# Kernel tuning notes

Measured on AMD Instinct MI355X. Metric: run time of the kernel, lower is better.

The kernel has to match this reference:

```python
import jax, jax.numpy as jnp
import numpy as np

VOCAB, HIDDEN, BATCH, SEQ = 32000, 512, 64, 512


def setup_inputs() -> dict:
    key = jax.random.key(0)
    k0, k1, k2, k3, k4, k5 = jax.random.split(key, 6)
    s = 1.0 / np.sqrt(HIDDEN)  # PyTorch LSTMCell init scale
    return {
        "inputs": jax.random.randint(k0, (BATCH, SEQ), 0, VOCAB, dtype=jnp.int64),
        "embedding": jax.random.normal(k1, (VOCAB, HIDDEN), dtype=jnp.float32),
        "W_ih": jax.random.normal(k2, (4 * HIDDEN, HIDDEN), dtype=jnp.float32) * s,
        "W_hh": jax.random.normal(k3, (4 * HIDDEN, HIDDEN), dtype=jnp.float32) * s,
        "b_ih": jax.random.normal(k4, (4 * HIDDEN,), dtype=jnp.float32) * s,
        "b_hh": jax.random.normal(k5, (4 * HIDDEN,), dtype=jnp.float32) * s,
    }


def reference(inputs, embedding, W_ih, W_hh, b_ih, b_hh):
    # Embedding lookup: (B, S, H)
    x = embedding[inputs]
    B, S, H = x.shape
    bias = b_ih + b_hh

    def step(carry, xt):
        h, c = carry
        # gates: (B, 4H); PyTorch LSTMCell gate order i, f, g, o
        gates = xt @ W_ih.T + h @ W_hh.T + bias
        i, f, g, o = jnp.split(gates, 4, axis=-1)
        i = jax.nn.sigmoid(i)
        f = jax.nn.sigmoid(f)
        g = jnp.tanh(g)
        o = jax.nn.sigmoid(o)
        c_new = f * c + i * g
        h_new = o * jnp.tanh(c_new)
        return (h_new, c_new), h_new

    h0 = jnp.zeros((B, H), dtype=x.dtype)
    c0 = jnp.zeros((B, H), dtype=x.dtype)
    (h, c), hs = jax.lax.scan(step, (h0, c0), jnp.swapaxes(x, 0, 1))
    annotations = jnp.swapaxes(hs, 0, 1)  # (B, S, H)
    return annotations, h, c
```

## Files before the change

kernel.cpp:

```cpp
#include <hip/hip_runtime.h>
#include <math.h>

#define B 64
#define S 512
#define H 512
#define G4 2048

typedef __attribute__((ext_vector_type(8))) short bf16x8;
typedef __attribute__((ext_vector_type(4))) float f32x4;

__device__ __forceinline__ float sigmoidf_(float x) {
    return 1.0f / (1.0f + __expf(-x));
}
__device__ __forceinline__ float tanhf_(float x) {
    return 2.0f / (1.0f + __expf(-2.0f * x)) - 1.0f;
}

__device__ __forceinline__ ushort f2bf(float f) {
    union { float f; unsigned int u; } v; v.f = f;
    unsigned int r = v.u + 0x7FFFu + ((v.u >> 16) & 1u);
    return (ushort)(r >> 16);
}
__device__ __forceinline__ float bf2f(ushort s) {
    union { unsigned int u; float f; } v; v.u = ((unsigned int)s) << 16;
    return v.f;
}
__device__ __forceinline__ void split_bf(float x, ushort& hi, ushort& lo) {
    const ushort h = f2bf(x);
    hi = h;
    lo = f2bf(x - bf2f(h));
}

__global__ __launch_bounds__(256)
void w_split(const float* __restrict__ W,
             ushort* __restrict__ Whi,
             ushort* __restrict__ Wlo)
{
    const int i = blockIdx.x * 256 + threadIdx.x;
    const float4 v = reinterpret_cast<const float4*>(W)[i];
    ushort4 hi, lo;
    split_bf(v.x, hi.x, lo.x);
    split_bf(v.y, hi.y, lo.y);
    split_bf(v.z, hi.z, lo.z);
    split_bf(v.w, hi.w, lo.w);
    reinterpret_cast<ushort4*>(Whi)[i] = hi;
    reinterpret_cast<ushort4*>(Wlo)[i] = lo;
}

__global__ __launch_bounds__(256)
void xg_mfma(const int* __restrict__ tokens,
             const float* __restrict__ emb,
             const ushort* __restrict__ Whi,
             const ushort* __restrict__ Wlo,
             const float* __restrict__ b_ih,
             const float* __restrict__ b_hh,
             ushort* __restrict__ xg)
{
    const int mtile = blockIdx.x;
    const int ntile = blockIdx.y;
    const int tid   = threadIdx.x;

    __shared__ ushort Ahi[128][32];
    __shared__ ushort Alo[128][32];
    __shared__ ushort Bhi[128][32];
    __shared__ ushort Blo[128][32];

    const int ar  = tid >> 3;
    const int seg = tid & 7;
    const float* asrc[4];
    #pragma unroll
    for (int i = 0; i < 4; ++i) {
        const int m   = mtile * 128 + ar + i * 32;
        const int tok = tokens[(m & 63) * S + (m >> 6)];
        asrc[i] = emb + (size_t)tok * H + seg * 4;
    }

    const int br = tid >> 2;
    const int bc = (tid & 3) * 8;
    const ushort* bsrc_hi[2];
    const ushort* bsrc_lo[2];
    #pragma unroll
    for (int j = 0; j < 2; ++j) {
        const int n = ntile * 128 + br + j * 64;
        bsrc_hi[j] = Whi + (size_t)n * H + bc;
        bsrc_lo[j] = Wlo + (size_t)n * H + bc;
    }

    const int lane = tid & 63;
    const int wv   = tid >> 6;
    const int wr   = (wv >> 1) * 64;
    const int wc   = (wv & 1) * 64;
    const int fr   = lane & 15;
    const int ks   = lane >> 4;

    f32x4 acc[4][4];
    #pragma unroll
    for (int a = 0; a < 4; ++a)
        #pragma unroll
        for (int c = 0; c < 4; ++c)
            acc[a][c] = (f32x4){0.f, 0.f, 0.f, 0.f};

    for (int kc = 0; kc < 16; ++kc) {
        const int d0 = kc * 32;

        #pragma unroll
        for (int i = 0; i < 4; ++i) {
            const float4 v = *reinterpret_cast<const float4*>(asrc[i] + d0);
            ushort4 hi, lo;
            split_bf(v.x, hi.x, lo.x);
            split_bf(v.y, hi.y, lo.y);
            split_bf(v.z, hi.z, lo.z);
            split_bf(v.w, hi.w, lo.w);
            const int r = ar + i * 32;
            *reinterpret_cast<ushort4*>(&Ahi[r][seg * 4]) = hi;
            *reinterpret_cast<ushort4*>(&Alo[r][seg * 4]) = lo;
        }
        #pragma unroll
        for (int j = 0; j < 2; ++j) {
            const int r = br + j * 64;
            *reinterpret_cast<uint4*>(&Bhi[r][bc]) =
                *reinterpret_cast<const uint4*>(bsrc_hi[j] + d0);
            *reinterpret_cast<uint4*>(&Blo[r][bc]) =
                *reinterpret_cast<const uint4*>(bsrc_lo[j] + d0);
        }
        __syncthreads();

        bf16x8 ah[4], al[4];
        #pragma unroll
        for (int fm = 0; fm < 4; ++fm) {
            ah[fm] = *reinterpret_cast<const bf16x8*>(&Ahi[wr + fm * 16 + fr][ks * 8]);
            al[fm] = *reinterpret_cast<const bf16x8*>(&Alo[wr + fm * 16 + fr][ks * 8]);
        }
        #pragma unroll
        for (int fn = 0; fn < 4; ++fn) {
            const bf16x8 bh = *reinterpret_cast<const bf16x8*>(&Bhi[wc + fn * 16 + fr][ks * 8]);
            const bf16x8 bl = *reinterpret_cast<const bf16x8*>(&Blo[wc + fn * 16 + fr][ks * 8]);
            #pragma unroll
            for (int fm = 0; fm < 4; ++fm) {
                acc[fm][fn] = __builtin_amdgcn_mfma_f32_16x16x32_bf16(ah[fm], bh, acc[fm][fn], 0, 0, 0);
                acc[fm][fn] = __builtin_amdgcn_mfma_f32_16x16x32_bf16(al[fm], bh, acc[fm][fn], 0, 0, 0);
                acc[fm][fn] = __builtin_amdgcn_mfma_f32_16x16x32_bf16(ah[fm], bl, acc[fm][fn], 0, 0, 0);
            }
        }
        __syncthreads();
    }

    #pragma unroll
    for (int fn = 0; fn < 4; ++fn) {
        const int col  = ntile * 128 + wc + fn * 16 + fr;
        const float bias = b_ih[col] + b_hh[col];
        const int gate = col >> 9;
        const int k    = col & 511;
        const int w    = k >> 4;
        const int kl   = k & 15;
        #pragma unroll
        for (int fm = 0; fm < 4; ++fm) {
            const int row = mtile * 128 + wr + fm * 16 + ks * 4;
            const int t   = row >> 6;
            const int b   = row & 63;
            const int g   = b >> 3;
            const int b8  = b & 7;
            ushort4 us;
            us.x = f2bf(acc[fm][fn][0] + bias);
            us.y = f2bf(acc[fm][fn][1] + bias);
            us.z = f2bf(acc[fm][fn][2] + bias);
            us.w = f2bf(acc[fm][fn][3] + bias);
            const size_t idx = ((((size_t)t * 8 + g) * 32 + w) * 512) +
                               gate * 128 + kl * 8 + b8;
            *reinterpret_cast<ushort4*>(&xg[idx]) = us;
        }
    }
}

__global__ __launch_bounds__(256)
void xg_gemm(const int* __restrict__ tokens,
             const float* __restrict__ emb,
             const float* __restrict__ W_ih,
             const float* __restrict__ b_ih,
             const float* __restrict__ b_hh,
             ushort* __restrict__ xg)
{
    const int t      = blockIdx.x;
    const int g_base = blockIdx.y * 128;
    const int tid    = threadIdx.x;

    const int b_ld = tid >> 2;
    const int seg  = tid & 3;
    const int r_w  = tid >> 1;
    const int half = tid & 1;
    const int b0 = (tid & 15) * 4;
    const int g0 = (tid >> 4) * 8;

    const int token = tokens[b_ld * S + t];
    const float4* embrow = reinterpret_cast<const float4*>(emb) + (size_t)token * (H / 4);

    __shared__ float hs[64][64];
    __shared__ float ws[128][68];

    float acc[4][8];
    #pragma unroll
    for (int i = 0; i < 4; ++i)
        #pragma unroll
        for (int j = 0; j < 8; ++j) acc[i][j] = 0.0f;

    for (int kc = 0; kc < 8; ++kc) {
        const int d0 = kc * 64;
        #pragma unroll
        for (int i = 0; i < 4; ++i) {
            const int dl = seg * 16 + i * 4;
            const float4 f = embrow[(d0 >> 2) + seg * 4 + i];
            hs[dl + 0][b_ld] = f.x;
            hs[dl + 1][b_ld] = f.y;
            hs[dl + 2][b_ld] = f.z;
            hs[dl + 3][b_ld] = f.w;
        }
        const float4* wrow = reinterpret_cast<const float4*>(W_ih) +
                             (size_t)(g_base + r_w) * (H / 4) + (d0 >> 2) + half * 8;
        #pragma unroll
        for (int i = 0; i < 8; ++i) {
            *reinterpret_cast<float4*>(&ws[r_w][half * 32 + i * 4]) = wrow[i];
        }
        __syncthreads();

        #pragma unroll
        for (int d4 = 0; d4 < 16; ++d4) {
            const float4 hv0 = *reinterpret_cast<const float4*>(&hs[d4 * 4 + 0][b0]);
            const float4 hv1 = *reinterpret_cast<const float4*>(&hs[d4 * 4 + 1][b0]);
            const float4 hv2 = *reinterpret_cast<const float4*>(&hs[d4 * 4 + 2][b0]);
            const float4 hv3 = *reinterpret_cast<const float4*>(&hs[d4 * 4 + 3][b0]);
            #pragma unroll
            for (int gg = 0; gg < 8; ++gg) {
                const float4 w = *reinterpret_cast<const float4*>(&ws[g0 + gg][d4 * 4]);
                acc[0][gg] += hv0.x * w.x + hv1.x * w.y + hv2.x * w.z + hv3.x * w.w;
                acc[1][gg] += hv0.y * w.x + hv1.y * w.y + hv2.y * w.z + hv3.y * w.w;
                acc[2][gg] += hv0.z * w.x + hv1.z * w.y + hv2.z * w.z + hv3.z * w.w;
                acc[3][gg] += hv0.w * w.x + hv1.w * w.y + hv2.w * w.z + hv3.w * w.w;
            }
        }
        __syncthreads();
    }

    const int grp = b0 >> 3;
    const int b8l = b0 & 7;
    #pragma unroll
    for (int gg = 0; gg < 8; ++gg) {
        const int gcol = g_base + g0 + gg;
        const int gate = gcol >> 9;
        const int k    = gcol & 511;
        const int w    = k >> 4;
        const int kl   = k & 15;
        const float bias = b_ih[gcol] + b_hh[gcol];
        ushort4 us;
        us.x = f2bf(acc[0][gg] + bias);
        us.y = f2bf(acc[1][gg] + bias);
        us.z = f2bf(acc[2][gg] + bias);
        us.w = f2bf(acc[3][gg] + bias);
        const size_t idx = ((((size_t)t * 8 + grp) * 32 + w) * 512) +
                           gate * 128 + kl * 8 + b8l;
        *reinterpret_cast<ushort4*>(&xg[idx]) = us;
    }
}

#define GSTR 4096
#define PSTR 32768

__global__ __launch_bounds__(256)
__attribute__((amdgpu_waves_per_eu(1, 1)))
void lstm_persist_mfma(const ushort* __restrict__ Whh_hi,
                       const ushort* __restrict__ Whh_lo,
                       const ushort* __restrict__ xg,
                       float* __restrict__ hq,
                       unsigned int* __restrict__ bar,
                       float* __restrict__ out)
{
    const int tid  = threadIdx.x;
    const int g    = blockIdx.x & 7;
    const int w    = blockIdx.x >> 3;
    const int k0   = w * 16;
    const int lane = tid & 63;
    const int wv   = tid >> 6;

    unsigned int* bcnt = bar + g * 64;

    const int  bcol   = lane & 15;
    const int  klane  = 4 * wv + (lane >> 4);
    const bool active = bcol < 8;
    const int  b8     = lane & 7;

    const ushort* xg_wg = xg + (((size_t)g * 32 + w) * 512);

    const int ar    = lane & 15;
    const int agate = ar & 3;
    const int ak    = k0 + 4 * wv + (ar >> 2);
    const size_t arow = ((size_t)agate * 512 + ak) * 512 + (size_t)(lane >> 4) * 8;
    bf16x8 afh[16], afl[16];
    #pragma unroll
    for (int ks = 0; ks < 16; ++ks) {
        afh[ks] = *reinterpret_cast<const bf16x8*>(Whh_hi + arow + ks * 32);
        afl[ks] = *reinterpret_cast<const bf16x8*>(Whh_lo + arow + ks * 32);
    }

    __shared__ ushort hs_hi[8 * 512];
    __shared__ ushort hs_lo[8 * 512];

    float c_reg = 0.0f;

    float xv_cur[4] = {0.f, 0.f, 0.f, 0.f};
    if (active) {
        #pragma unroll
        for (int gate = 0; gate < 4; ++gate)
            xv_cur[gate] = bf2f(xg_wg[gate * 128 + klane * 8 + b8]);
    }

    char* hs_hi_c = reinterpret_cast<char*>(hs_hi);
    char* hs_lo_c = reinterpret_cast<char*>(hs_lo);

    for (int t = 0; t < S; ++t) {
        const unsigned long long* hsrc8 = reinterpret_cast<const unsigned long long*>(
            hq + (t & 1) * PSTR + g * GSTR);
        unsigned long long hv[8];
        #pragma unroll
        for (int i = 0; i < 8; ++i)
            hv[i] = __hip_atomic_load(&hsrc8[i * 256 + tid],
                                      __ATOMIC_RELAXED, __HIP_MEMORY_SCOPE_AGENT);
        #pragma unroll
        for (int i = 0; i < 8; ++i) {
            const int e  = 2 * (i * 256 + tid);
            const int bb = e >> 9;
            const int dd = e & 511;
            union { unsigned long long u; float f[2]; } uv; uv.u = hv[i];
            ushort h0, l0, h1, l1;
            split_bf(uv.f[0], h0, l0);
            split_bf(uv.f[1], h1, l1);
            const int byteoff = ((bb << 10) + (dd << 1)) ^ (bb << 4);
            *reinterpret_cast<unsigned int*>(hs_hi_c + byteoff) =
                ((unsigned int)h1 << 16) | (unsigned int)h0;
            *reinterpret_cast<unsigned int*>(hs_lo_c + byteoff) =
                ((unsigned int)l1 << 16) | (unsigned int)l0;
        }
        __syncthreads();

        float xv_nxt[4] = {0.f, 0.f, 0.f, 0.f};
        if (active && t + 1 < S) {
            const ushort* p = xg_wg + (size_t)(t + 1) * (8 * 32 * 512);
            #pragma unroll
            for (int gate = 0; gate < 4; ++gate)
                xv_nxt[gate] = bf2f(p[gate * 128 + klane * 8 + b8]);
        }

        f32x4 a0 = (f32x4){0.f,0.f,0.f,0.f}, a1 = a0, a2 = a0, a3 = a0, a4 = a0, a5 = a0;
        #pragma unroll
        for (int ks = 0; ks < 16; ++ks) {
            const int kbyte = ((b8 << 10) + ((ks * 32 + (lane >> 4) * 8) << 1)) ^ (b8 << 4);
            const bf16x8 bh = *reinterpret_cast<const bf16x8*>(hs_hi_c + kbyte);
            const bf16x8 bl = *reinterpret_cast<const bf16x8*>(hs_lo_c + kbyte);
            if (ks & 1) {
                a1 = __builtin_amdgcn_mfma_f32_16x16x32_bf16(afh[ks], bh, a1, 0, 0, 0);
                a3 = __builtin_amdgcn_mfma_f32_16x16x32_bf16(afl[ks], bh, a3, 0, 0, 0);
                a5 = __builtin_amdgcn_mfma_f32_16x16x32_bf16(afh[ks], bl, a5, 0, 0, 0);
            } else {
                a0 = __builtin_amdgcn_mfma_f32_16x16x32_bf16(afh[ks], bh, a0, 0, 0, 0);
                a2 = __builtin_amdgcn_mfma_f32_16x16x32_bf16(afl[ks], bh, a2, 0, 0, 0);
                a4 = __builtin_amdgcn_mfma_f32_16x16x32_bf16(afh[ks], bl, a4, 0, 0, 0);
            }
        }
        const f32x4 acc = (a0 + a1) + ((a2 + a3) + (a4 + a5));

        float hn = 0.0f, cn = 0.0f;
        if (active) {
            const float ig = sigmoidf_(acc[0] + xv_cur[0]);
            const float fg = sigmoidf_(acc[1] + xv_cur[1]);
            const float gg = tanhf_(acc[2] + xv_cur[2]);
            const float og = sigmoidf_(acc[3] + xv_cur[3]);
            cn = fg * c_reg + ig * gg;
            c_reg = cn;
            hn = og * tanhf_(cn);
            __hip_atomic_store(&hq[((t & 1) ^ 1) * PSTR + g * GSTR + b8 * 512 + k0 + klane],
                               hn, __ATOMIC_RELAXED, __HIP_MEMORY_SCOPE_AGENT);
        }

        __syncthreads();
        if (tid == 0)
            __hip_atomic_fetch_add(bcnt, 1u, __ATOMIC_RELAXED,
                                   __HIP_MEMORY_SCOPE_AGENT);

        if (active) {
            out[((size_t)(g * 8 + b8) * S + t) * H + k0 + klane] = hn;
            if (t == S - 1) {
                const size_t OFF = (size_t)B * S * H;
                out[OFF + (size_t)(g * 8 + b8) * H + k0 + klane] = hn;
                out[OFF + (size_t)B * H + (size_t)(g * 8 + b8) * H + k0 + klane] = cn;
            }
        }

        const unsigned int target = 32u * (unsigned int)(t + 1);
        while (__hip_atomic_load(bcnt, __ATOMIC_RELAXED,
                                 __HIP_MEMORY_SCOPE_AGENT) < target)
            __builtin_amdgcn_s_sleep(2);

        xv_cur[0] = xv_nxt[0]; xv_cur[1] = xv_nxt[1];
        xv_cur[2] = xv_nxt[2]; xv_cur[3] = xv_nxt[3];
    }
}

__global__ __launch_bounds__(256)
__attribute__((amdgpu_waves_per_eu(1, 1)))
void lstm_persist(const float* __restrict__ W_hh,
                  const ushort* __restrict__ xg,
                  float* __restrict__ hq,
                  unsigned int* __restrict__ bar,
                  float* __restrict__ out)
{
    const int tid = threadIdx.x;
    const int g   = blockIdx.x & 7;
    const int w   = blockIdx.x >> 3;
    const int k0  = w * 16;

    const int rp = tid & 31;
    const int d8 = tid >> 5;
    const int d0 = d8 * 64;

    const int b8 = tid >> 4;
    const int kl = tid & 15;

    unsigned int* bcnt = bar + g * 64;

    const ushort* xg_wg = xg + (((size_t)g * 32 + w) * 512);

    float4 wreg[2][16];
    #pragma unroll
    for (int r = 0; r < 2; ++r) {
        const int rl = 2 * rp + r;
        const int grow = (rl >> 4) * H + k0 + (rl & 15);
        const float4* wp = reinterpret_cast<const float4*>(W_hh + (size_t)grow * H + d0);
        #pragma unroll
        for (int i = 0; i < 16; ++i) wreg[r][i] = wp[i];
    }

    __shared__ float hs[8 * 512];
    __shared__ float part[8 * 8 * 64];

    float c_reg = 0.0f;

    float xv_cur[4] = {0.f, 0.f, 0.f, 0.f};
    if (tid < 128) {
        #pragma unroll
        for (int gate = 0; gate < 4; ++gate)
            xv_cur[gate] = bf2f(xg_wg[gate * 128 + kl * 8 + b8]);
    }

    for (int t = 0; t < S; ++t) {
        const unsigned long long* hsrc8 = reinterpret_cast<const unsigned long long*>(
            hq + (t & 1) * PSTR + g * GSTR);
        #pragma unroll
        for (int i = 0; i < 8; ++i) {
            const unsigned long long v = __hip_atomic_load(&hsrc8[i * 256 + tid],
                                                           __ATOMIC_RELAXED,
                                                           __HIP_MEMORY_SCOPE_AGENT);
            reinterpret_cast<unsigned long long*>(hs)[i * 256 + tid] = v;
        }
        __syncthreads();

        float xv_nxt[4] = {0.f, 0.f, 0.f, 0.f};
        if (tid < 128 && t + 1 < S) {
            const ushort* p = xg_wg + (size_t)(t + 1) * (8 * 32 * 512);
            #pragma unroll
            for (int gate = 0; gate < 4; ++gate)
                xv_nxt[gate] = bf2f(p[gate * 128 + kl * 8 + b8]);
        }

        float acc[2][8];
        #pragma unroll
        for (int r = 0; r < 2; ++r)
            #pragma unroll
            for (int b = 0; b < 8; ++b) acc[r][b] = 0.0f;

        #pragma unroll
        for (int b = 0; b < 8; ++b) {
            const float4* h4 = reinterpret_cast<const float4*>(hs + b * 512 + d0);
            #pragma unroll
            for (int i = 0; i < 16; ++i) {
                const float4 hv = h4[i];
                acc[0][b] += wreg[0][i].x * hv.x + wreg[0][i].y * hv.y +
                             wreg[0][i].z * hv.z + wreg[0][i].w * hv.w;
                acc[1][b] += wreg[1][i].x * hv.x + wreg[1][i].y * hv.y +
                             wreg[1][i].z * hv.z + wreg[1][i].w * hv.w;
            }
        }

        #pragma unroll
        for (int r = 0; r < 2; ++r)
            #pragma unroll
            for (int b = 0; b < 8; ++b)
                part[d8 * 512 + b * 64 + 2 * rp + r] = acc[r][b];
        __syncthreads();

        if (tid < 128) {
            float v[4];
            #pragma unroll
            for (int gate = 0; gate < 4; ++gate) {
                const int rl = gate * 16 + kl;
                float s = 0.0f;
                #pragma unroll
                for (int q = 0; q < 8; ++q) s += part[q * 512 + b8 * 64 + rl];
                v[gate] = s + xv_cur[gate];
            }
            const float ig = sigmoidf_(v[0]);
            const float fg = sigmoidf_(v[1]);
            const float gg = tanhf_(v[2]);
            const float og = sigmoidf_(v[3]);

            const float cn = fg * c_reg + ig * gg;
            c_reg = cn;
            const float hn = og * tanhf_(cn);

            __hip_atomic_store(&hq[((t & 1) ^ 1) * PSTR + g * GSTR + b8 * 512 + k0 + kl],
                               hn, __ATOMIC_RELAXED, __HIP_MEMORY_SCOPE_AGENT);
            out[((size_t)(g * 8 + b8) * S + t) * H + k0 + kl] = hn;
            if (t == S - 1) {
                const size_t OFF = (size_t)B * S * H;
                out[OFF + (size_t)(g * 8 + b8) * H + k0 + kl] = hn;
                out[OFF + (size_t)B * H + (size_t)(g * 8 + b8) * H + k0 + kl] = cn;
            }
        }

        __syncthreads();
        if (tid == 0) {
            __hip_atomic_fetch_add(bcnt, 1u, __ATOMIC_RELAXED,
                                   __HIP_MEMORY_SCOPE_AGENT);
            const unsigned int target = 32u * (unsigned int)(t + 1);
            while (__hip_atomic_load(bcnt, __ATOMIC_RELAXED,
                                     __HIP_MEMORY_SCOPE_AGENT) < target)
                __builtin_amdgcn_s_sleep(2);
        }
        __syncthreads();

        xv_cur[0] = xv_nxt[0]; xv_cur[1] = xv_nxt[1];
        xv_cur[2] = xv_nxt[2]; xv_cur[3] = xv_nxt[3];
    }
}

__global__ __launch_bounds__(128)
void lstm_step_fb(const int* __restrict__ tokens,
                  const float* __restrict__ emb,
                  const float* __restrict__ W_ih,
                  const float* __restrict__ W_hh,
                  const float* __restrict__ b_ih,
                  const float* __restrict__ b_hh,
                  const float* __restrict__ h_prev,
                  float* __restrict__ h_next,
                  float* __restrict__ c_st,
                  float* __restrict__ out,
                  int t)
{
    const int tid = threadIdx.x;
    const int b   = tid & 63;
    const int k   = blockIdx.x * 2 + (tid >> 6);
    const int token = tokens[b * S + t];
    const float* xrow = emb + (size_t)token * H;
    const float* hrow = h_prev + b * H;
    float acc[4];
    #pragma unroll
    for (int g = 0; g < 4; ++g) acc[g] = b_ih[g * H + k] + b_hh[g * H + k];
    for (int d = 0; d < H; ++d) {
        const float xv = xrow[d], hv = hrow[d];
        #pragma unroll
        for (int g = 0; g < 4; ++g)
            acc[g] += xv * W_ih[(size_t)(g * H + k) * H + d] + hv * W_hh[(size_t)(g * H + k) * H + d];
    }
    const float ig = sigmoidf_(acc[0]);
    const float fg = sigmoidf_(acc[1]);
    const float gg = tanhf(acc[2]);
    const float og = sigmoidf_(acc[3]);
    const int ck = b * H + k;
    const float cn = fg * c_st[ck] + ig * gg;
    c_st[ck] = cn;
    const float hn = og * tanhf(cn);
    h_next[ck] = hn;
    out[(size_t)b * S * H + (size_t)t * H + k] = hn;
    if (t == S - 1) {
        out[(size_t)B * S * H + ck] = hn;
        out[(size_t)B * S * H + B * H + ck] = cn;
    }
}

extern "C" void kernel_launch(void* const* d_in, const int* in_sizes, int n_in,
                              void* d_out, int out_size, void* d_ws, size_t ws_size,
                              hipStream_t stream)
{
    const int*   tokens = (const int*)d_in[0];
    const float* emb    = (const float*)d_in[1];
    const float* W_ih   = (const float*)d_in[2];
    const float* W_hh   = (const float*)d_in[3];
    const float* b_ih   = (const float*)d_in[4];
    const float* b_hh   = (const float*)d_in[5];
    float* out = (float*)d_out;

    const size_t XG_BYTES  = (size_t)S * G4 * B * 2;
    const size_t HQ_BYTES  = (size_t)2 * PSTR * 4;
    const size_t BAR_BYTES = 8 * 64 * 4;
    const size_t W_BYTES   = (size_t)G4 * H * 2;
    const size_t NEED_OLD  = XG_BYTES + HQ_BYTES + BAR_BYTES;
    const size_t NEED_R1   = NEED_OLD + 2 * W_BYTES;
    const size_t NEED_R2   = NEED_OLD + 4 * W_BYTES;

    if (ws_size >= NEED_R2) {
        ushort* xg = (ushort*)d_ws;
        float*  hq = (float*)((char*)d_ws + XG_BYTES);
        unsigned int* bar = (unsigned int*)((char*)d_ws + XG_BYTES + HQ_BYTES);
        ushort* Wih_hi = (ushort*)((char*)d_ws + NEED_OLD);
        ushort* Wih_lo = Wih_hi + (size_t)G4 * H;
        ushort* Whh_hi = Wih_lo + (size_t)G4 * H;
        ushort* Whh_lo = Whh_hi + (size_t)G4 * H;

        (void)hipMemsetAsync(hq, 0, HQ_BYTES + BAR_BYTES, stream);

        w_split<<<dim3((G4 * H / 4) / 256), dim3(256), 0, stream>>>(W_ih, Wih_hi, Wih_lo);
        w_split<<<dim3((G4 * H / 4) / 256), dim3(256), 0, stream>>>(W_hh, Whh_hi, Whh_lo);

        xg_mfma<<<dim3(256, 16), dim3(256), 0, stream>>>(
            tokens, emb, Wih_hi, Wih_lo, b_ih, b_hh, xg);

        lstm_persist_mfma<<<dim3(256), dim3(256), 0, stream>>>(
            Whh_hi, Whh_lo, xg, hq, bar, out);
    } else if (ws_size >= NEED_R1) {
        ushort* xg = (ushort*)d_ws;
        float*  hq = (float*)((char*)d_ws + XG_BYTES);
        unsigned int* bar = (unsigned int*)((char*)d_ws + XG_BYTES + HQ_BYTES);
        ushort* Wih_hi = (ushort*)((char*)d_ws + NEED_OLD);
        ushort* Wih_lo = Wih_hi + (size_t)G4 * H;

        (void)hipMemsetAsync(hq, 0, HQ_BYTES + BAR_BYTES, stream);

        w_split<<<dim3((G4 * H / 4) / 256), dim3(256), 0, stream>>>(W_ih, Wih_hi, Wih_lo);

        xg_mfma<<<dim3(256, 16), dim3(256), 0, stream>>>(
            tokens, emb, Wih_hi, Wih_lo, b_ih, b_hh, xg);

        lstm_persist<<<dim3(256), dim3(256), 0, stream>>>(W_hh, xg, hq, bar, out);
    } else if (ws_size >= NEED_OLD) {
        ushort* xg = (ushort*)d_ws;
        float*  hq = (float*)((char*)d_ws + XG_BYTES);
        unsigned int* bar = (unsigned int*)((char*)d_ws + XG_BYTES + HQ_BYTES);

        (void)hipMemsetAsync(hq, 0, HQ_BYTES + BAR_BYTES, stream);

        xg_gemm<<<dim3(S, 16), dim3(256), 0, stream>>>(tokens, emb, W_ih, b_ih, b_hh, xg);

        lstm_persist<<<dim3(256), dim3(256), 0, stream>>>(W_hh, xg, hq, bar, out);
    } else {
        float* c_st = (float*)d_ws;
        float* h0   = c_st + B * H;
        float* h1   = h0 + B * H;
        (void)hipMemsetAsync(d_ws, 0, (size_t)3 * B * H * sizeof(float), stream);
        for (int t = 0; t < S; ++t) {
            const float* hp = (t & 1) ? h1 : h0;
            float*       hn = (t & 1) ? h0 : h1;
            lstm_step_fb<<<dim3(256), dim3(128), 0, stream>>>(
                tokens, emb, W_ih, W_hh, b_ih, b_hh, hp, hn, c_st, out, t);
        }
    }
}
```

Before: 1.972 ms.

## Replace counter barrier with per-wave flags and publish pre-split bf16 hidden state

The persistent LSTM kernel no longer uses a per-group atomic counter barrier with __syncthreads. Instead each wave writes its own step flag, and consumers poll all 128 flags of their group with one wave-wide load. Producers now store the hidden state already split into hi/lo bf16 in the swizzled LDS layout, so consumers copy it straight into shared memory without converting. This aims to cut barrier latency and per-step conversion work. The cost is more polling traffic and relaxed-ordering visibility that depends on s_waitcnt. The other fallback paths now share the changed hq/flag sizes.

```diff
diff --git a/kernel.cpp b/kernel.cpp
--- a/kernel.cpp
+++ b/kernel.cpp
@@ -263,15 +263,17 @@
 
 #define GSTR 4096
 #define PSTR 32768
+#define HQG  16384
+#define HQP  (8 * HQG)
 
 __global__ __launch_bounds__(256)
 __attribute__((amdgpu_waves_per_eu(1, 1)))
-void lstm_persist_mfma(const ushort* __restrict__ Whh_hi,
-                       const ushort* __restrict__ Whh_lo,
-                       const ushort* __restrict__ xg,
-                       float* __restrict__ hq,
-                       unsigned int* __restrict__ bar,
-                       float* __restrict__ out)
+void lstm_persist_mfma2(const ushort* __restrict__ Whh_hi,
+                        const ushort* __restrict__ Whh_lo,
+                        const ushort* __restrict__ xg,
+                        char* __restrict__ hq,
+                        unsigned int* __restrict__ flags,
+                        float* __restrict__ out)
 {
     const int tid  = threadIdx.x;
     const int g    = blockIdx.x & 7;
@@ -280,8 +282,6 @@
     const int lane = tid & 63;
     const int wv   = tid >> 6;
 
-    unsigned int* bcnt = bar + g * 64;
-
     const int  bcol   = lane & 15;
     const int  klane  = 4 * wv + (lane >> 4);
     const bool active = bcol < 8;
@@ -300,8 +300,7 @@
         afl[ks] = *reinterpret_cast<const bf16x8*>(Whh_lo + arow + ks * 32);
     }
 
-    __shared__ ushort hs_hi[8 * 512];
-    __shared__ ushort hs_lo[8 * 512];
+    __shared__ char hsB[HQG];
 
     float c_reg = 0.0f;
 
@@ -312,32 +311,32 @@
             xv_cur[gate] = bf2f(xg_wg[gate * 128 + klane * 8 + b8]);
     }
 
-    char* hs_hi_c = reinterpret_cast<char*>(hs_hi);
-    char* hs_lo_c = reinterpret_cast<char*>(hs_lo);
+    const unsigned long long* fgrp =
+        reinterpret_cast<const unsigned long long*>(flags + g * 128);
+    unsigned int* myflag = flags + g * 128 + (w * 4 + wv);
 
     for (int t = 0; t < S; ++t) {
-        const unsigned long long* hsrc8 = reinterpret_cast<const unsigned long long*>(
-            hq + (t & 1) * PSTR + g * GSTR);
+        for (;;) {
+            const unsigned long long fv =
+                __hip_atomic_load(&fgrp[lane], __ATOMIC_RELAXED,
+                                  __HIP_MEMORY_SCOPE_AGENT);
+            if (__all(((unsigned int)fv >= (unsigned int)t) &&
+                      ((unsigned int)(fv >> 32) >= (unsigned int)t)))
+                break;
+            __builtin_amdgcn_s_sleep(1);
+        }
+        asm volatile("" ::: "memory");
+
+        const unsigned long long* hsrc = reinterpret_cast<const unsigned long long*>(
+            hq + (size_t)(t & 1) * HQP + (size_t)g * HQG);
         unsigned long long hv[8];
         #pragma unroll
         for (int i = 0; i < 8; ++i)
-            hv[i] = __hip_atomic_load(&hsrc8[i * 256 + tid],
+            hv[i] = __hip_atomic_load(&hsrc[i * 256 + tid],
                                       __ATOMIC_RELAXED, __HIP_MEMORY_SCOPE_AGENT);
         #pragma unroll
-        for (int i = 0; i < 8; ++i) {
-            const int e  = 2 * (i * 256 + tid);
-            const int bb = e >> 9;
-            const int dd = e & 511;
-            union { unsigned long long u; float f[2]; } uv; uv.u = hv[i];
-            ushort h0, l0, h1, l1;
-            split_bf(uv.f[0], h0, l0);
-            split_bf(uv.f[1], h1, l1);
-            const int byteoff = ((bb << 10) + (dd << 1)) ^ (bb << 4);
-            *reinterpret_cast<unsigned int*>(hs_hi_c + byteoff) =
-                ((unsigned int)h1 << 16) | (unsigned int)h0;
-            *reinterpret_cast<unsigned int*>(hs_lo_c + byteoff) =
-                ((unsigned int)l1 << 16) | (unsigned int)l0;
-        }
+        for (int i = 0; i < 8; ++i)
+            *reinterpret_cast<unsigned long long*>(hsB + (i * 256 + tid) * 8) = hv[i];
         __syncthreads();
 
         float xv_nxt[4] = {0.f, 0.f, 0.f, 0.f};
@@ -352,8 +351,8 @@
         #pragma unroll
         for (int ks = 0; ks < 16; ++ks) {
             const int kbyte = ((b8 << 10) + ((ks * 32 + (lane >> 4) * 8) << 1)) ^ (b8 << 4);
-            const bf16x8 bh = *reinterpret_cast<const bf16x8*>(hs_hi_c + kbyte);
-            const bf16x8 bl = *reinterpret_cast<const bf16x8*>(hs_lo_c + kbyte);
+            const bf16x8 bh = *reinterpret_cast<const bf16x8*>(hsB + kbyte);
+            const bf16x8 bl = *reinterpret_cast<const bf16x8*>(hsB + 8192 + kbyte);
             if (ks & 1) {
                 a1 = __builtin_amdgcn_mfma_f32_16x16x32_bf16(afh[ks], bh, a1, 0, 0, 0);
                 a3 = __builtin_amdgcn_mfma_f32_16x16x32_bf16(afl[ks], bh, a3, 0, 0, 0);
@@ -375,14 +374,21 @@
             cn = fg * c_reg + ig * gg;
             c_reg = cn;
             hn = og * tanhf_(cn);
-            __hip_atomic_store(&hq[((t & 1) ^ 1) * PSTR + g * GSTR + b8 * 512 + k0 + klane],
-                               hn, __ATOMIC_RELAXED, __HIP_MEMORY_SCOPE_AGENT);
-        }
-
-        __syncthreads();
-        if (tid == 0)
-            __hip_atomic_fetch_add(bcnt, 1u, __ATOMIC_RELAXED,
-                                   __HIP_MEMORY_SCOPE_AGENT);
+
+            char* hqw = hq + (size_t)((t & 1) ^ 1) * HQP + (size_t)g * HQG;
+            const int f = ((b8 << 10) + ((k0 + klane) << 1)) ^ (b8 << 4);
+            ushort hh, hl;
+            split_bf(hn, hh, hl);
+            __hip_atomic_store(reinterpret_cast<ushort*>(hqw + f), hh,
+                               __ATOMIC_RELAXED, __HIP_MEMORY_SCOPE_AGENT);
+            __hip_atomic_store(reinterpret_cast<ushort*>(hqw + 8192 + f), hl,
+                               __ATOMIC_RELAXED, __HIP_MEMORY_SCOPE_AGENT);
+        }
+
+        asm volatile("s_waitcnt vmcnt(0)" ::: "memory");
+        if (lane == 0)
+            __hip_atomic_store(myflag, (unsigned int)(t + 1),
+                               __ATOMIC_RELAXED, __HIP_MEMORY_SCOPE_AGENT);
 
         if (active) {
             out[((size_t)(g * 8 + b8) * S + t) * H + k0 + klane] = hn;
@@ -392,11 +398,6 @@
                 out[OFF + (size_t)B * H + (size_t)(g * 8 + b8) * H + k0 + klane] = cn;
             }
         }
-
-        const unsigned int target = 32u * (unsigned int)(t + 1);
-        while (__hip_atomic_load(bcnt, __ATOMIC_RELAXED,
-                                 __HIP_MEMORY_SCOPE_AGENT) < target)
-            __builtin_amdgcn_s_sleep(2);
 
         xv_cur[0] = xv_nxt[0]; xv_cur[1] = xv_nxt[1];
         xv_cur[2] = xv_nxt[2]; xv_cur[3] = xv_nxt[3];
@@ -596,24 +597,24 @@
     const float* b_hh   = (const float*)d_in[5];
     float* out = (float*)d_out;
 
-    const size_t XG_BYTES  = (size_t)S * G4 * B * 2;
-    const size_t HQ_BYTES  = (size_t)2 * PSTR * 4;
-    const size_t BAR_BYTES = 8 * 64 * 4;
-    const size_t W_BYTES   = (size_t)G4 * H * 2;
-    const size_t NEED_OLD  = XG_BYTES + HQ_BYTES + BAR_BYTES;
-    const size_t NEED_R1   = NEED_OLD + 2 * W_BYTES;
-    const size_t NEED_R2   = NEED_OLD + 4 * W_BYTES;
+    const size_t XG_BYTES   = (size_t)S * G4 * B * 2;
+    const size_t HQ_BYTES   = (size_t)2 * HQP;
+    const size_t FLAG_BYTES = 4096;
+    const size_t W_BYTES    = (size_t)G4 * H * 2;
+    const size_t NEED_OLD   = XG_BYTES + HQ_BYTES + FLAG_BYTES;
+    const size_t NEED_R1    = NEED_OLD + 2 * W_BYTES;
+    const size_t NEED_R2    = NEED_OLD + 4 * W_BYTES;
 
     if (ws_size >= NEED_R2) {
         ushort* xg = (ushort*)d_ws;
-        float*  hq = (float*)((char*)d_ws + XG_BYTES);
-        unsigned int* bar = (unsigned int*)((char*)d_ws + XG_BYTES + HQ_BYTES);
+        char*   hq = (char*)d_ws + XG_BYTES;
+        unsigned int* flags = (unsigned int*)((char*)d_ws + XG_BYTES + HQ_BYTES);
         ushort* Wih_hi = (ushort*)((char*)d_ws + NEED_OLD);
         ushort* Wih_lo = Wih_hi + (size_t)G4 * H;
         ushort* Whh_hi = Wih_lo + (size_t)G4 * H;
         ushort* Whh_lo = Whh_hi + (size_t)G4 * H;
 
-        (void)hipMemsetAsync(hq, 0, HQ_BYTES + BAR_BYTES, stream);
+        (void)hipMemsetAsync(hq, 0, HQ_BYTES + FLAG_BYTES, stream);
 
         w_split<<<dim3((G4 * H / 4) / 256), dim3(256), 0, stream>>>(W_ih, Wih_hi, Wih_lo);
         w_split<<<dim3((G4 * H / 4) / 256), dim3(256), 0, stream>>>(W_hh, Whh_hi, Whh_lo);
@@ -621,8 +622,8 @@
         xg_mfma<<<dim3(256, 16), dim3(256), 0, stream>>>(
             tokens, emb, Wih_hi, Wih_lo, b_ih, b_hh, xg);
 
-        lstm_persist_mfma<<<dim3(256), dim3(256), 0, stream>>>(
-            Whh_hi, Whh_lo, xg, hq, bar, out);
+        lstm_persist_mfma2<<<dim3(256), dim3(256), 0, stream>>>(
+            Whh_hi, Whh_lo, xg, hq, flags, out);
     } else if (ws_size >= NEED_R1) {
         ushort* xg = (ushort*)d_ws;
         float*  hq = (float*)((char*)d_ws + XG_BYTES);
@@ -630,7 +631,7 @@
         ushort* Wih_hi = (ushort*)((char*)d_ws + NEED_OLD);
         ushort* Wih_lo = Wih_hi + (size_t)G4 * H;
 
-        (void)hipMemsetAsync(hq, 0, HQ_BYTES + BAR_BYTES, stream);
+        (void)hipMemsetAsync(hq, 0, HQ_BYTES + FLAG_BYTES, stream);
 
         w_split<<<dim3((G4 * H / 4) / 256), dim3(256), 0, stream>>>(W_ih, Wih_hi, Wih_lo);
 
@@ -643,7 +644,7 @@
         float*  hq = (float*)((char*)d_ws + XG_BYTES);
         unsigned int* bar = (unsigned int*)((char*)d_ws + XG_BYTES + HQ_BYTES);
 
-        (void)hipMemsetAsync(hq, 0, HQ_BYTES + BAR_BYTES, stream);
+        (void)hipMemsetAsync(hq, 0, HQ_BYTES + FLAG_BYTES, stream);
 
         xg_gemm<<<dim3(S, 16), dim3(256), 0, stream>>>(tokens, emb, W_ih, b_ih, b_hh, xg);
 
```

New measurement: 5.000 ms. 2.54x slower.

## Replace shared atomic counter barrier with per-block flag array and wave-wide polling

Applied to the files above, without the earlier changes.

Swaps the per-group fetch-add counter barrier for per-workgroup step flags. Each block stores t+1 to its own padded flag after producing h, and at the start of the next step polls all 32 peer flags in parallel across lanes with __all. The aim is to remove atomic contention on a single counter and move the wait to just before h is needed, so output stores overlap with the wait. Memory ordering now relies only on relaxed atomics plus a compiler barrier, which risks visibility races for the h values.

```diff
diff --git a/kernel.cpp b/kernel.cpp
--- a/kernel.cpp
+++ b/kernel.cpp
@@ -266,12 +266,12 @@
 
 __global__ __launch_bounds__(256)
 __attribute__((amdgpu_waves_per_eu(1, 1)))
-void lstm_persist_mfma(const ushort* __restrict__ Whh_hi,
-                       const ushort* __restrict__ Whh_lo,
-                       const ushort* __restrict__ xg,
-                       float* __restrict__ hq,
-                       unsigned int* __restrict__ bar,
-                       float* __restrict__ out)
+void lstm_persist_mfma3(const ushort* __restrict__ Whh_hi,
+                        const ushort* __restrict__ Whh_lo,
+                        const ushort* __restrict__ xg,
+                        float* __restrict__ hq,
+                        unsigned int* __restrict__ flags,
+                        float* __restrict__ out)
 {
     const int tid  = threadIdx.x;
     const int g    = blockIdx.x & 7;
@@ -280,8 +280,6 @@
     const int lane = tid & 63;
     const int wv   = tid >> 6;
 
-    unsigned int* bcnt = bar + g * 64;
-
     const int  bcol   = lane & 15;
     const int  klane  = 4 * wv + (lane >> 4);
     const bool active = bcol < 8;
@@ -315,7 +313,19 @@
     char* hs_hi_c = reinterpret_cast<char*>(hs_hi);
     char* hs_lo_c = reinterpret_cast<char*>(hs_lo);
 
+    unsigned int* fgrp  = flags + g * 512;
+    unsigned int* myflg = fgrp + w * 16;
+    const int     pidx  = (lane & 31) * 16;
+
     for (int t = 0; t < S; ++t) {
+        for (;;) {
+            const unsigned int fv = __hip_atomic_load(&fgrp[pidx], __ATOMIC_RELAXED,
+                                                      __HIP_MEMORY_SCOPE_AGENT);
+            if (__all(fv >= (unsigned int)t)) break;
+            __builtin_amdgcn_s_sleep(1);
+        }
+        asm volatile("" ::: "memory");
+
         const unsigned long long* hsrc8 = reinterpret_cast<const unsigned long long*>(
             hq + (t & 1) * PSTR + g * GSTR);
         unsigned long long hv[8];
@@ -381,8 +391,8 @@
 
         __syncthreads();
         if (tid == 0)
-            __hip_atomic_fetch_add(bcnt, 1u, __ATOMIC_RELAXED,
-                                   __HIP_MEMORY_SCOPE_AGENT);
+            __hip_atomic_store(myflg, (unsigned int)(t + 1),
+                               __ATOMIC_RELAXED, __HIP_MEMORY_SCOPE_AGENT);
 
         if (active) {
             out[((size_t)(g * 8 + b8) * S + t) * H + k0 + klane] = hn;
@@ -392,11 +402,6 @@
                 out[OFF + (size_t)B * H + (size_t)(g * 8 + b8) * H + k0 + klane] = cn;
             }
         }
-
-        const unsigned int target = 32u * (unsigned int)(t + 1);
-        while (__hip_atomic_load(bcnt, __ATOMIC_RELAXED,
-                                 __HIP_MEMORY_SCOPE_AGENT) < target)
-            __builtin_amdgcn_s_sleep(2);
 
         xv_cur[0] = xv_nxt[0]; xv_cur[1] = xv_nxt[1];
         xv_cur[2] = xv_nxt[2]; xv_cur[3] = xv_nxt[3];
@@ -596,24 +601,24 @@
     const float* b_hh   = (const float*)d_in[5];
     float* out = (float*)d_out;
 
-    const size_t XG_BYTES  = (size_t)S * G4 * B * 2;
-    const size_t HQ_BYTES  = (size_t)2 * PSTR * 4;
-    const size_t BAR_BYTES = 8 * 64 * 4;
-    const size_t W_BYTES   = (size_t)G4 * H * 2;
-    const size_t NEED_OLD  = XG_BYTES + HQ_BYTES + BAR_BYTES;
-    const size_t NEED_R1   = NEED_OLD + 2 * W_BYTES;
-    const size_t NEED_R2   = NEED_OLD + 4 * W_BYTES;
+    const size_t XG_BYTES   = (size_t)S * G4 * B * 2;
+    const size_t HQ_BYTES   = (size_t)2 * PSTR * 4;
+    const size_t FLAG_BYTES = 16384;
+    const size_t W_BYTES    = (size_t)G4 * H * 2;
+    const size_t NEED_OLD   = XG_BYTES + HQ_BYTES + FLAG_BYTES;
+    const size_t NEED_R1    = NEED_OLD + 2 * W_BYTES;
+    const size_t NEED_R2    = NEED_OLD + 4 * W_BYTES;
 
     if (ws_size >= NEED_R2) {
         ushort* xg = (ushort*)d_ws;
         float*  hq = (float*)((char*)d_ws + XG_BYTES);
-        unsigned int* bar = (unsigned int*)((char*)d_ws + XG_BYTES + HQ_BYTES);
+        unsigned int* flags = (unsigned int*)((char*)d_ws + XG_BYTES + HQ_BYTES);
         ushort* Wih_hi = (ushort*)((char*)d_ws + NEED_OLD);
         ushort* Wih_lo = Wih_hi + (size_t)G4 * H;
         ushort* Whh_hi = Wih_lo + (size_t)G4 * H;
         ushort* Whh_lo = Whh_hi + (size_t)G4 * H;
 
-        (void)hipMemsetAsync(hq, 0, HQ_BYTES + BAR_BYTES, stream);
+        (void)hipMemsetAsync(hq, 0, HQ_BYTES + FLAG_BYTES, stream);
 
         w_split<<<dim3((G4 * H / 4) / 256), dim3(256), 0, stream>>>(W_ih, Wih_hi, Wih_lo);
         w_split<<<dim3((G4 * H / 4) / 256), dim3(256), 0, stream>>>(W_hh, Whh_hi, Whh_lo);
@@ -621,8 +626,8 @@
         xg_mfma<<<dim3(256, 16), dim3(256), 0, stream>>>(
             tokens, emb, Wih_hi, Wih_lo, b_ih, b_hh, xg);
 
-        lstm_persist_mfma<<<dim3(256), dim3(256), 0, stream>>>(
-            Whh_hi, Whh_lo, xg, hq, bar, out);
+        lstm_persist_mfma3<<<dim3(256), dim3(256), 0, stream>>>(
+            Whh_hi, Whh_lo, xg, hq, flags, out);
     } else if (ws_size >= NEED_R1) {
         ushort* xg = (ushort*)d_ws;
         float*  hq = (float*)((char*)d_ws + XG_BYTES);
@@ -630,7 +635,7 @@
         ushort* Wih_hi = (ushort*)((char*)d_ws + NEED_OLD);
         ushort* Wih_lo = Wih_hi + (size_t)G4 * H;
 
-        (void)hipMemsetAsync(hq, 0, HQ_BYTES + BAR_BYTES, stream);
+        (void)hipMemsetAsync(hq, 0, HQ_BYTES + FLAG_BYTES, stream);
 
         w_split<<<dim3((G4 * H / 4) / 256), dim3(256), 0, stream>>>(W_ih, Wih_hi, Wih_lo);
 
@@ -643,7 +648,7 @@
         float*  hq = (float*)((char*)d_ws + XG_BYTES);
         unsigned int* bar = (unsigned int*)((char*)d_ws + XG_BYTES + HQ_BYTES);
 
-        (void)hipMemsetAsync(hq, 0, HQ_BYTES + BAR_BYTES, stream);
+        (void)hipMemsetAsync(hq, 0, HQ_BYTES + FLAG_BYTES, stream);
 
         xg_gemm<<<dim3(S, 16), dim3(256), 0, stream>>>(tokens, emb, W_ih, b_ih, b_hh, xg);
 
```

Result: slower. 2.134 ms (+8.2%).
